# Kernel tuning notes

Hardware: AMD Instinct MI355X
Metric: run time of the kernel (lower is better)

## Reference

```python
import jax, jax.numpy as jnp
import numpy as np

B, L, DIM, H, D = 2, 2048, 1024, 16, 64


def setup_inputs() -> dict:
    key = jax.random.key(0)
    ks = jax.random.split(key, 20)
    s = 1.0 / np.sqrt(DIM)
    inp = {
        "query": jax.random.normal(ks[0], (B, L, DIM), jnp.float32),
        "keys": jax.random.normal(ks[1], (B, L, DIM), jnp.float32),
        "values": jax.random.normal(ks[2], (B, L, DIM), jnp.float32),
        "focus_vector": jax.random.normal(ks[3], (B, DIM), jnp.float32),
        "temporal_weights": jax.random.normal(ks[4], (B, L), jnp.float32),
        "importance_weights": jax.random.normal(ks[5], (B, L), jnp.float32),
        # linear params, stored [in, out] for x @ W + b
        "Wq": jax.random.normal(ks[6], (DIM, H * D), jnp.float32) * s,
        "bq": jnp.zeros((H * D,), jnp.float32),
        "Wk": jax.random.normal(ks[7], (DIM, H * D), jnp.float32) * s,
        "bk": jnp.zeros((H * D,), jnp.float32),
        "Wv": jax.random.normal(ks[8], (DIM, H * D), jnp.float32) * s,
        "bv": jnp.zeros((H * D,), jnp.float32),
        "Wp": jax.random.normal(ks[9], (H * D, DIM), jnp.float32) * s,
        "bp": jnp.zeros((DIM,), jnp.float32),
        "Wt": jax.random.normal(ks[10], (DIM, 1), jnp.float32) * s,
        "bt": jnp.zeros((1,), jnp.float32),
        "Wi": jax.random.normal(ks[11], (DIM, 1), jnp.float32) * s,
        "bi": jnp.zeros((1,), jnp.float32),
    }
    return inp


def reference(query, keys, values, focus_vector, temporal_weights, importance_weights,
              Wq, bq, Wk, bk, Wv, bv, Wp, bp, Wt, bt, Wi, bi):
    b, l, _ = query.shape
    # QKV projections -> [B, H, L, D]
    q = (query @ Wq + bq).reshape(b, l, H, D).transpose(0, 2, 1, 3)
    k = (keys @ Wk + bk).reshape(b, -1, H, D).transpose(0, 2, 1, 3)
    v = (values @ Wv + bv).reshape(b, -1, H, D).transpose(0, 2, 1, 3)
    scores = jnp.einsum("bhqd,bhkd->bhqk", q, k) / np.sqrt(D).astype(np.float32)
    # gate-modulated weights over keys [B, Lk]
    temporal_scores = (keys @ Wt + bt)[..., 0]
    tw = jax.nn.softmax(temporal_scores * temporal_weights, axis=-1)
    importance_scores = (keys @ Wi + bi)[..., 0]
    iw = jax.nn.softmax(importance_scores * importance_weights, axis=-1)
    rw = jax.nn.softmax(jnp.einsum("bkd,bd->bk", keys, focus_vector), axis=-1)
    combined = (tw + iw + rw) / 3.0
    scores = scores * combined[:, None, None, :]
    weights = jax.nn.softmax(scores, axis=-1)  # dropout is identity in eval
    out = jnp.einsum("bhqk,bhkd->bhqd", weights, v)
    out = out.transpose(0, 2, 1, 3).reshape(b, l, H * D)
    out = out @ Wp + bp
    return out, weights
```

## Files before the change

kernel.cpp:

```cpp
#include <hip/hip_runtime.h>
#include <hip/hip_bf16.h>
#include <cstdint>

#define DEV static __device__ __forceinline__

typedef __attribute__((ext_vector_type(8))) short short8_;
typedef __attribute__((ext_vector_type(4))) float float4_;
typedef __attribute__((ext_vector_type(4))) float f4v;
typedef __attribute__((ext_vector_type(4))) unsigned short u16x4;
typedef unsigned short u16;

constexpr int Bb   = 2;
constexpr int Ls   = 2048;
constexpr int DIMc = 1024;
constexpr int Hh   = 16;
constexpr int Dd   = 64;
constexpr int BL   = Bb * Ls;
constexpr int HD   = Hh * Dd;

DEV u16 f2bf(float f) {
  union { float f; uint32_t u; } v; v.f = f;
  return (u16)((v.u + 0x7fffu + ((v.u >> 16) & 1u)) >> 16);
}

DEV float4_ mfma16(short8_ a, short8_ b, float4_ c) {
  return __builtin_amdgcn_mfma_f32_16x16x32_bf16(a, b, c, 0, 0, 0);
}

DEV void gload_lds16(const void* g, void* l) {
  __builtin_amdgcn_global_load_lds(
      (const __attribute__((address_space(1))) void*)g,
      (__attribute__((address_space(3))) void*)l, 16, 0, 0);
}

__global__ void k_cast(const float* __restrict__ src, u16* __restrict__ dst, int n4) {
  int i = blockIdx.x * 256 + threadIdx.x;
  if (i >= n4) return;
  f4v v = ((const f4v*)src)[i];
  u16x4 o = { f2bf(v[0]), f2bf(v[1]), f2bf(v[2]), f2bf(v[3]) };
  ((u16x4*)dst)[i] = o;
}

__global__ void k_trans(const float* __restrict__ W, u16* __restrict__ WT) {
  __shared__ float t[64][65];
  int tx = threadIdx.x & 63;
  int tg = threadIdx.x >> 6;
  int n0 = blockIdx.x * 64;
  int k0 = blockIdx.y * 64;
#pragma unroll
  for (int i = 0; i < 16; ++i) {
    int r = tg * 16 + i;
    t[r][tx] = W[(size_t)(k0 + r) * HD + n0 + tx];
  }
  __syncthreads();
#pragma unroll
  for (int i = 0; i < 16; ++i) {
    int r = tg * 16 + i;
    WT[(size_t)(n0 + r) * DIMc + k0 + tx] = f2bf(t[tx][r]);
  }
}

__global__ void k_gates(const float* __restrict__ keys, const float* __restrict__ Wt,
                        const float* __restrict__ bt, const float* __restrict__ Wi,
                        const float* __restrict__ bi, const float* __restrict__ focus,
                        float* __restrict__ ts, float* __restrict__ is_, float* __restrict__ rs) {
  int wv = threadIdx.x >> 6, ln = threadIdx.x & 63;
  int row = blockIdx.x * 4 + wv;
  int b = row >> 11;
  const float* kr = keys + (size_t)row * DIMc;
  const float* fr = focus + (size_t)b * DIMc;
  float st = 0.f, si = 0.f, sr = 0.f;
  for (int j = ln; j < DIMc; j += 64) {
    float kv = kr[j];
    st += kv * Wt[j]; si += kv * Wi[j]; sr += kv * fr[j];
  }
#pragma unroll
  for (int m = 1; m < 64; m <<= 1) {
    st += __shfl_xor(st, m); si += __shfl_xor(si, m); sr += __shfl_xor(sr, m);
  }
  if (ln == 0) { ts[row] = st + bt[0]; is_[row] = si + bi[0]; rs[row] = sr; }
}

__global__ void k_combined(const float* __restrict__ ts, const float* __restrict__ is_,
                           const float* __restrict__ rs, const float* __restrict__ tw,
                           const float* __restrict__ iw, float* __restrict__ comb) {
  int b = blockIdx.x, t = threadIdx.x;
  __shared__ float red[3][4];
  float lt[8], li[8], lr[8];
  float m3[3] = {-1e30f, -1e30f, -1e30f};
#pragma unroll
  for (int i = 0; i < 8; ++i) {
    int gi = b * Ls + i * 256 + t;
    lt[i] = ts[gi] * tw[gi];
    li[i] = is_[gi] * iw[gi];
    lr[i] = rs[gi];
    m3[0] = fmaxf(m3[0], lt[i]); m3[1] = fmaxf(m3[1], li[i]); m3[2] = fmaxf(m3[2], lr[i]);
  }
#pragma unroll
  for (int q = 0; q < 3; ++q) {
    float v = m3[q];
#pragma unroll
    for (int m = 32; m; m >>= 1) v = fmaxf(v, __shfl_xor(v, m));
    if ((t & 63) == 0) red[q][t >> 6] = v;
  }
  __syncthreads();
#pragma unroll
  for (int q = 0; q < 3; ++q)
    m3[q] = fmaxf(fmaxf(red[q][0], red[q][1]), fmaxf(red[q][2], red[q][3]));
  __syncthreads();
  float s3[3] = {0.f, 0.f, 0.f};
#pragma unroll
  for (int i = 0; i < 8; ++i) {
    lt[i] = __expf(lt[i] - m3[0]); s3[0] += lt[i];
    li[i] = __expf(li[i] - m3[1]); s3[1] += li[i];
    lr[i] = __expf(lr[i] - m3[2]); s3[2] += lr[i];
  }
#pragma unroll
  for (int q = 0; q < 3; ++q) {
    float v = s3[q];
#pragma unroll
    for (int m = 32; m; m >>= 1) v += __shfl_xor(v, m);
    if ((t & 63) == 0) red[q][t >> 6] = v;
  }
  __syncthreads();
#pragma unroll
  for (int q = 0; q < 3; ++q) s3[q] = red[q][0] + red[q][1] + red[q][2] + red[q][3];
  float rt = 1.f / s3[0], ri = 1.f / s3[1], rr = 1.f / s3[2];
  const float third = 1.f / 3.f;
#pragma unroll
  for (int i = 0; i < 8; ++i) {
    int gi = b * Ls + i * 256 + t;
    comb[gi] = (lt[i] * rt + li[i] * ri + lr[i] * rr) * third;
  }
}

template <int MODE>
__launch_bounds__(256, 2)
__global__ void k_gemm(const u16* __restrict__ A, const u16* __restrict__ BT,
                       const float* __restrict__ bias, void* __restrict__ out) {
  __shared__ __align__(16) u16 As[128 * 32];
  __shared__ __align__(16) u16 Bs[128 * 32];
  const int tid = threadIdx.x, wv = tid >> 6, ln = tid & 63;
  const int g = ln >> 4, c = ln & 15;
  const int m0 = blockIdx.x * 128, n0 = blockIdx.y * 128;
  const int wm = wv >> 1, wn = wv & 1;
  const float4_ z4 = {0.f, 0.f, 0.f, 0.f};
  float4_ acc[4][4];
#pragma unroll
  for (int i = 0; i < 4; ++i)
#pragma unroll
    for (int j = 0; j < 4; ++j) acc[i][j] = z4;
  const int lrow = ln >> 2, lcol = (ln & 3) * 8;
  for (int k0 = 0; k0 < 1024; k0 += 32) {
#pragma unroll
    for (int s = 0; s < 2; ++s) {
      int r0 = wv * 32 + s * 16;
      gload_lds16(A  + (size_t)(m0 + r0 + lrow) * 1024 + k0 + lcol, &As[r0 * 32]);
      gload_lds16(BT + (size_t)(n0 + r0 + lrow) * 1024 + k0 + lcol, &Bs[r0 * 32]);
    }
    __syncthreads();
    short8_ af[4], bfr[4];
#pragma unroll
    for (int mt = 0; mt < 4; ++mt)
      af[mt] = *(const short8_*)&As[(wm * 64 + mt * 16 + c) * 32 + g * 8];
#pragma unroll
    for (int nt = 0; nt < 4; ++nt)
      bfr[nt] = *(const short8_*)&Bs[(wn * 64 + nt * 16 + c) * 32 + g * 8];
#pragma unroll
    for (int mt = 0; mt < 4; ++mt)
#pragma unroll
      for (int nt = 0; nt < 4; ++nt)
        acc[mt][nt] = mfma16(af[mt], bfr[nt], acc[mt][nt]);
    __syncthreads();
  }
  if constexpr (MODE == 3) {
    float* O = (float*)out;
#pragma unroll
    for (int mt = 0; mt < 4; ++mt)
#pragma unroll
      for (int nt = 0; nt < 4; ++nt) {
        int n = n0 + wn * 64 + nt * 16 + c;
        float bv = bias[n];
#pragma unroll
        for (int r = 0; r < 4; ++r) {
          int m = m0 + wm * 64 + mt * 16 + g * 4 + r;
          O[(size_t)m * HD + n] = acc[mt][nt][r] + bv;
        }
      }
  } else if constexpr (MODE == 2) {
    u16* vT = (u16*)out;
#pragma unroll
    for (int mt = 0; mt < 4; ++mt)
#pragma unroll
      for (int nt = 0; nt < 4; ++nt) {
        int n = n0 + wn * 64 + nt * 16 + c;
        float bv = bias[n];
        int h = n >> 6, d = n & 63;
        int mrow = m0 + wm * 64 + mt * 16 + g * 4;
        int b = mrow >> 11, l = mrow & 2047;
        u16x4 o = { f2bf(acc[mt][nt][0] + bv), f2bf(acc[mt][nt][1] + bv),
                    f2bf(acc[mt][nt][2] + bv), f2bf(acc[mt][nt][3] + bv) };
        *(u16x4*)&vT[((size_t)((b * Hh + h) * Dd + d)) * Ls + l] = o;
      }
  } else {
    u16* Q = (u16*)out;
#pragma unroll
    for (int mt = 0; mt < 4; ++mt)
#pragma unroll
      for (int nt = 0; nt < 4; ++nt) {
        int n = n0 + wn * 64 + nt * 16 + c;
        float bv = bias[n];
        int h = n >> 6, d = n & 63;
#pragma unroll
        for (int r = 0; r < 4; ++r) {
          int m = m0 + wm * 64 + mt * 16 + g * 4 + r;
          int b = m >> 11, l = m & 2047;
          Q[((size_t)((b * Hh + h) * Ls + l)) * Dd + d] = f2bf(acc[mt][nt][r] + bv);
        }
      }
  }
}

__launch_bounds__(256, 3)
__global__ void k_attn2(const u16* __restrict__ q_bh, const u16* __restrict__ k_bh,
                        const u16* __restrict__ vT, const float* __restrict__ comb_g,
                        float* __restrict__ wout, u16* __restrict__ ctx) {
  __shared__ __align__(16) u16 Kt[2][64][64];
  __shared__ __align__(16) u16 Vt[2][64][64];
  __shared__ float comb[Ls];
  __shared__ __align__(16) u16 e_w[4][16][72];
  __shared__ float inv_w[4][16];

  const int bid = blockIdx.x;
  const int logical = (bid & 7) * 128 + (bid >> 3);
  const int bh = logical >> 5, qb = logical & 31;
  const int b = bh >> 4, h = bh & 15;
  const int l0 = qb * 64;
  const int w = threadIdx.x >> 6, ln = threadIdx.x & 63;
  const int g = ln >> 4, c = ln & 15;
  const int srow = ln >> 3, x8 = ln & 7;
  const float4_ z4 = {0.f, 0.f, 0.f, 0.f};

  const u16* kbh = k_bh + (size_t)bh * Ls * Dd;
  const u16* vbh = vT + (size_t)bh * Dd * Ls;

  const u16* qp = q_bh + ((size_t)bh * Ls + l0 + w * 16) * Dd;
  short8_ aq0 = *(const short8_*)&qp[c * Dd + g * 8];
  short8_ aq1 = *(const short8_*)&qp[c * Dd + 32 + g * 8];

  auto stageK = [&](int buf, int kb) {
#pragma unroll
    for (int i = 0; i < 2; ++i) {
      int rr = w * 16 + i * 8 + srow;
      int sc = (x8 ^ (rr & 7)) * 8;
      gload_lds16(kbh + (size_t)(kb + rr) * Dd + sc, &Kt[buf][w * 16 + i * 8][0]);
    }
  };
  auto stageV = [&](int buf, int kb) {
#pragma unroll
    for (int i = 0; i < 2; ++i) {
      int rr = w * 16 + i * 8 + srow;
      int sc = (x8 ^ (rr & 7)) * 8;
      gload_lds16(vbh + (size_t)rr * Ls + kb + sc, &Vt[buf][w * 16 + i * 8][0]);
    }
  };

  float4_ accO[4];
#pragma unroll
  for (int dt = 0; dt < 4; ++dt) accO[dt] = z4;
  float rsum4[4] = {0.f, 0.f, 0.f, 0.f};

  stageK(0, 0); stageV(0, 0);
  for (int i = threadIdx.x; i < Ls; i += 256) comb[i] = comb_g[b * Ls + i] * 0.125f;
  __syncthreads();

  int buf = 0;
  for (int t = 0; t < 32; ++t) {
    if (t < 31) { stageK(buf ^ 1, (t + 1) * 64); stageV(buf ^ 1, (t + 1) * 64); }
    const int kb = t * 64;
#pragma unroll
    for (int s = 0; s < 4; ++s) {
      int rowK = s * 16 + c;
      short8_ bk0 = *(const short8_*)&Kt[buf][rowK][((g    ) ^ (c & 7)) * 8];
      short8_ bk1 = *(const short8_*)&Kt[buf][rowK][((4 + g) ^ (c & 7)) * 8];
      float4_ st = mfma16(aq0, bk0, z4);
      st = mfma16(aq1, bk1, st);
      float cc = comb[kb + rowK];
#pragma unroll
      for (int r = 0; r < 4; ++r) {
        float e = __expf(st[r] * cc);
        rsum4[r] += e;
        e_w[w][g * 4 + r][s * 16 + c] = f2bf(e);
      }
    }
#pragma unroll
    for (int hf = 0; hf < 2; ++hf) {
      short8_ ea = *(const short8_*)&e_w[w][c][hf * 32 + g * 8];
#pragma unroll
      for (int dt = 0; dt < 4; ++dt) {
        short8_ bv = *(const short8_*)&Vt[buf][dt * 16 + c][((hf * 4 + g) ^ (c & 7)) * 8];
        accO[dt] = mfma16(ea, bv, accO[dt]);
      }
    }
    __syncthreads();
    buf ^= 1;
  }

#pragma unroll
  for (int m = 1; m < 16; m <<= 1)
#pragma unroll
    for (int r = 0; r < 4; ++r) rsum4[r] += __shfl_xor(rsum4[r], m);
  float invr[4];
#pragma unroll
  for (int r = 0; r < 4; ++r) invr[r] = 1.0f / rsum4[r];
  if (c == 0)
#pragma unroll
    for (int r = 0; r < 4; ++r) inv_w[w][g * 4 + r] = invr[r];

  u16* out_lds = &Vt[0][0][0] + w * 1152;
#pragma unroll
  for (int dt = 0; dt < 4; ++dt)
#pragma unroll
    for (int r = 0; r < 4; ++r)
      out_lds[(g * 4 + r) * 72 + dt * 16 + c] = f2bf(accO[dt][r] * invr[r]);
  {
    int rr2 = ln >> 2, sg = ln & 3;
    short8_ d0 = *(const short8_*)&out_lds[rr2 * 72 + sg * 16];
    short8_ d1 = *(const short8_*)&out_lds[rr2 * 72 + sg * 16 + 8];
    u16* cp = ctx + ((size_t)(b * Ls + l0 + w * 16 + rr2)) * HD + h * Dd + sg * 16;
    *(short8_*)cp = d0;
    *(short8_*)(cp + 8) = d1;
  }

  float ivq = inv_w[w][c];
  stageK(0, 0);
  __syncthreads();
  buf = 0;
  float* wb = wout + ((size_t)bh * Ls + l0 + w * 16) * Ls;
  for (int t = 0; t < 32; ++t) {
    if (t < 31) stageK(buf ^ 1, (t + 1) * 64);
    const int kb = t * 64;
#pragma unroll
    for (int s = 0; s < 4; ++s) {
      int rowK = s * 16 + c;
      short8_ bk0 = *(const short8_*)&Kt[buf][rowK][((g    ) ^ (c & 7)) * 8];
      short8_ bk1 = *(const short8_*)&Kt[buf][rowK][((4 + g) ^ (c & 7)) * 8];
      float4_ st = mfma16(bk0, aq0, z4);
      st = mfma16(bk1, aq1, st);
      float4_ cc4 = *(const float4_*)&comb[kb + s * 16 + g * 4];
      float4_ o;
#pragma unroll
      for (int r = 0; r < 4; ++r) o[r] = __expf(st[r] * cc4[r]) * ivq;
      *(float4_*)&wb[(size_t)c * Ls + kb + s * 16 + g * 4] = o;
    }
    __syncthreads();
    buf ^= 1;
  }
}

extern "C" void kernel_launch(void* const* d_in, const int* in_sizes, int n_in,
                              void* d_out, int out_size, void* d_ws, size_t ws_size,
                              hipStream_t stream) {
  (void)in_sizes; (void)n_in; (void)out_size; (void)ws_size;
  const float* query = (const float*)d_in[0];
  const float* keys  = (const float*)d_in[1];
  const float* values= (const float*)d_in[2];
  const float* focus = (const float*)d_in[3];
  const float* twg   = (const float*)d_in[4];
  const float* iwg   = (const float*)d_in[5];
  const float* Wq = (const float*)d_in[6];  const float* bq = (const float*)d_in[7];
  const float* Wk = (const float*)d_in[8];  const float* bk = (const float*)d_in[9];
  const float* Wv = (const float*)d_in[10]; const float* bv = (const float*)d_in[11];
  const float* Wp = (const float*)d_in[12]; const float* bp = (const float*)d_in[13];
  const float* Wt = (const float*)d_in[14]; const float* bt = (const float*)d_in[15];
  const float* Wi = (const float*)d_in[16]; const float* bi = (const float*)d_in[17];

  char* ws = (char*)d_ws;
  size_t off = 0;
  auto alloc = [&](size_t bytes) -> char* {
    char* p = ws + off; off += (bytes + 255) & ~(size_t)255; return p;
  };
  const size_t NTOK = (size_t)BL * DIMc;
  u16* qx   = (u16*)alloc(NTOK * 2);
  u16* kx   = (u16*)alloc(NTOK * 2);
  u16* vx   = (u16*)alloc(NTOK * 2);
  u16* WqT  = (u16*)alloc((size_t)DIMc * HD * 2);
  u16* WkT  = (u16*)alloc((size_t)DIMc * HD * 2);
  u16* WvT  = (u16*)alloc((size_t)DIMc * HD * 2);
  u16* WpT  = (u16*)alloc((size_t)DIMc * HD * 2);
  u16* q_bh = (u16*)alloc(NTOK * 2);
  u16* k_bh = (u16*)alloc(NTOK * 2);
  u16* vTb  = (u16*)alloc(NTOK * 2);
  u16* ctx  = (u16*)alloc(NTOK * 2);
  float* ts   = (float*)alloc((size_t)BL * 4);
  float* is_  = (float*)alloc((size_t)BL * 4);
  float* rs   = (float*)alloc((size_t)BL * 4);
  float* comb = (float*)alloc((size_t)BL * 4);

  float* out_f = (float*)d_out;
  float* w_out = out_f + (size_t)BL * HD;

  const int n4 = (int)(NTOK / 4);
  k_cast<<<4096, 256, 0, stream>>>(query,  qx, n4);
  k_cast<<<4096, 256, 0, stream>>>(keys,   kx, n4);
  k_cast<<<4096, 256, 0, stream>>>(values, vx, n4);
  dim3 tg(16, 16);
  k_trans<<<tg, 256, 0, stream>>>(Wq, WqT);
  k_trans<<<tg, 256, 0, stream>>>(Wk, WkT);
  k_trans<<<tg, 256, 0, stream>>>(Wv, WvT);
  k_trans<<<tg, 256, 0, stream>>>(Wp, WpT);
  k_gates<<<1024, 256, 0, stream>>>(keys, Wt, bt, Wi, bi, focus, ts, is_, rs);
  k_combined<<<2, 256, 0, stream>>>(ts, is_, rs, twg, iwg, comb);
  dim3 gg(32, 8);
  k_gemm<0><<<gg, 256, 0, stream>>>(qx, WqT, bq, q_bh);
  k_gemm<0><<<gg, 256, 0, stream>>>(kx, WkT, bk, k_bh);
  k_gemm<2><<<gg, 256, 0, stream>>>(vx, WvT, bv, vTb);
  k_attn2<<<1024, 256, 0, stream>>>(q_bh, k_bh, vTb, comb, w_out, ctx);
  k_gemm<3><<<gg, 256, 0, stream>>>(ctx, WpT, bp, out_f);
}
```

Baseline: 341.5 us.

## Batch cast, transpose and QKV GEMM launches; trim attention LDS and swizzle

New measurement: 297.6 us. 12.9% less time.

```diff
diff --git a/kernel.cpp b/kernel.cpp
--- a/kernel.cpp
+++ b/kernel.cpp
@@ -33,16 +33,26 @@
       (__attribute__((address_space(3))) void*)l, 16, 0, 0);
 }
 
-__global__ void k_cast(const float* __restrict__ src, u16* __restrict__ dst, int n4) {
+__global__ void k_cast3(const float* __restrict__ a, const float* __restrict__ b,
+                        const float* __restrict__ c, u16* __restrict__ oa,
+                        u16* __restrict__ ob, u16* __restrict__ oc) {
+  int z = blockIdx.y;
+  const float* s = (z == 0) ? a : (z == 1) ? b : c;
+  u16* d = (z == 0) ? oa : (z == 1) ? ob : oc;
   int i = blockIdx.x * 256 + threadIdx.x;
-  if (i >= n4) return;
-  f4v v = ((const f4v*)src)[i];
+  f4v v = ((const f4v*)s)[i];
   u16x4 o = { f2bf(v[0]), f2bf(v[1]), f2bf(v[2]), f2bf(v[3]) };
-  ((u16x4*)dst)[i] = o;
-}
-
-__global__ void k_trans(const float* __restrict__ W, u16* __restrict__ WT) {
+  ((u16x4*)d)[i] = o;
+}
+
+__global__ void k_trans4(const float* __restrict__ W0, const float* __restrict__ W1,
+                         const float* __restrict__ W2, const float* __restrict__ W3,
+                         u16* __restrict__ T0, u16* __restrict__ T1,
+                         u16* __restrict__ T2, u16* __restrict__ T3) {
   __shared__ float t[64][65];
+  int z = blockIdx.z;
+  const float* W = (z == 0) ? W0 : (z == 1) ? W1 : (z == 2) ? W2 : W3;
+  u16* WT = (z == 0) ? T0 : (z == 1) ? T1 : (z == 2) ? T2 : T3;
   int tx = threadIdx.x & 63;
   int tg = threadIdx.x >> 6;
   int n0 = blockIdx.x * 64;
@@ -126,20 +136,27 @@
 #pragma unroll
   for (int q = 0; q < 3; ++q) s3[q] = red[q][0] + red[q][1] + red[q][2] + red[q][3];
   float rt = 1.f / s3[0], ri = 1.f / s3[1], rr = 1.f / s3[2];
-  const float third = 1.f / 3.f;
+  const float scl = (1.f / 3.f) * 0.125f;
 #pragma unroll
   for (int i = 0; i < 8; ++i) {
     int gi = b * Ls + i * 256 + t;
-    comb[gi] = (lt[i] * rt + li[i] * ri + lr[i] * rr) * third;
-  }
-}
-
-template <int MODE>
+    comb[gi] = (lt[i] * rt + li[i] * ri + lr[i] * rr) * scl;
+  }
+}
+
 __launch_bounds__(256, 2)
-__global__ void k_gemm(const u16* __restrict__ A, const u16* __restrict__ BT,
-                       const float* __restrict__ bias, void* __restrict__ out) {
+__global__ void k_gemm_qkv(const u16* __restrict__ qx, const u16* __restrict__ kx,
+                           const u16* __restrict__ vx, const u16* __restrict__ WqT,
+                           const u16* __restrict__ WkT, const u16* __restrict__ WvT,
+                           const float* __restrict__ bq, const float* __restrict__ bk,
+                           const float* __restrict__ bv, u16* __restrict__ q_bh,
+                           u16* __restrict__ k_bh, u16* __restrict__ vT) {
   __shared__ __align__(16) u16 As[128 * 32];
   __shared__ __align__(16) u16 Bs[128 * 32];
+  const int z = blockIdx.z;
+  const u16* A  = (z == 0) ? qx : (z == 1) ? kx : vx;
+  const u16* BT = (z == 0) ? WqT : (z == 1) ? WkT : WvT;
+  const float* bias = (z == 0) ? bq : (z == 1) ? bk : bv;
   const int tid = threadIdx.x, wv = tid >> 6, ln = tid & 63;
   const int g = ln >> 4, c = ln & 15;
   const int m0 = blockIdx.x * 128, n0 = blockIdx.y * 128;
@@ -173,63 +190,98 @@
         acc[mt][nt] = mfma16(af[mt], bfr[nt], acc[mt][nt]);
     __syncthreads();
   }
-  if constexpr (MODE == 3) {
-    float* O = (float*)out;
+  if (z < 2) {
+    u16* Q = (z == 0) ? q_bh : k_bh;
 #pragma unroll
     for (int mt = 0; mt < 4; ++mt)
 #pragma unroll
       for (int nt = 0; nt < 4; ++nt) {
         int n = n0 + wn * 64 + nt * 16 + c;
-        float bv = bias[n];
+        float bv_ = bias[n];
+        int h = n >> 6, d = n & 63;
 #pragma unroll
         for (int r = 0; r < 4; ++r) {
           int m = m0 + wm * 64 + mt * 16 + g * 4 + r;
-          O[(size_t)m * HD + n] = acc[mt][nt][r] + bv;
+          int b = m >> 11, l = m & 2047;
+          Q[((size_t)((b * Hh + h) * Ls + l)) * Dd + d] = f2bf(acc[mt][nt][r] + bv_);
         }
       }
-  } else if constexpr (MODE == 2) {
-    u16* vT = (u16*)out;
+  } else {
 #pragma unroll
     for (int mt = 0; mt < 4; ++mt)
 #pragma unroll
       for (int nt = 0; nt < 4; ++nt) {
         int n = n0 + wn * 64 + nt * 16 + c;
-        float bv = bias[n];
+        float bv_ = bias[n];
         int h = n >> 6, d = n & 63;
         int mrow = m0 + wm * 64 + mt * 16 + g * 4;
         int b = mrow >> 11, l = mrow & 2047;
-        u16x4 o = { f2bf(acc[mt][nt][0] + bv), f2bf(acc[mt][nt][1] + bv),
-                    f2bf(acc[mt][nt][2] + bv), f2bf(acc[mt][nt][3] + bv) };
+        u16x4 o = { f2bf(acc[mt][nt][0] + bv_), f2bf(acc[mt][nt][1] + bv_),
+                    f2bf(acc[mt][nt][2] + bv_), f2bf(acc[mt][nt][3] + bv_) };
         *(u16x4*)&vT[((size_t)((b * Hh + h) * Dd + d)) * Ls + l] = o;
       }
-  } else {
-    u16* Q = (u16*)out;
-#pragma unroll
-    for (int mt = 0; mt < 4; ++mt)
-#pragma unroll
-      for (int nt = 0; nt < 4; ++nt) {
-        int n = n0 + wn * 64 + nt * 16 + c;
-        float bv = bias[n];
-        int h = n >> 6, d = n & 63;
-#pragma unroll
-        for (int r = 0; r < 4; ++r) {
-          int m = m0 + wm * 64 + mt * 16 + g * 4 + r;
-          int b = m >> 11, l = m & 2047;
-          Q[((size_t)((b * Hh + h) * Ls + l)) * Dd + d] = f2bf(acc[mt][nt][r] + bv);
-        }
+  }
+}
+
+__launch_bounds__(256, 4)
+__global__ void k_gemmO(const u16* __restrict__ A, const u16* __restrict__ BT,
+                        const float* __restrict__ bias, float* __restrict__ O) {
+  __shared__ __align__(16) u16 As[64 * 32];
+  __shared__ __align__(16) u16 Bs[128 * 32];
+  const int tid = threadIdx.x, wv = tid >> 6, ln = tid & 63;
+  const int g = ln >> 4, c = ln & 15;
+  const int m0 = blockIdx.x * 64, n0 = blockIdx.y * 128;
+  const int wm = wv >> 1, wn = wv & 1;
+  const float4_ z4 = {0.f, 0.f, 0.f, 0.f};
+  float4_ acc[2][4];
+#pragma unroll
+  for (int i = 0; i < 2; ++i)
+#pragma unroll
+    for (int j = 0; j < 4; ++j) acc[i][j] = z4;
+  const int lrow = ln >> 2, lcol = (ln & 3) * 8;
+  for (int k0 = 0; k0 < 1024; k0 += 32) {
+    gload_lds16(A + (size_t)(m0 + wv * 16 + lrow) * 1024 + k0 + lcol, &As[(wv * 16) * 32]);
+#pragma unroll
+    for (int s = 0; s < 2; ++s) {
+      int r0 = wv * 32 + s * 16;
+      gload_lds16(BT + (size_t)(n0 + r0 + lrow) * 1024 + k0 + lcol, &Bs[r0 * 32]);
+    }
+    __syncthreads();
+    short8_ af[2], bfr[4];
+#pragma unroll
+    for (int mt = 0; mt < 2; ++mt)
+      af[mt] = *(const short8_*)&As[(wm * 32 + mt * 16 + c) * 32 + g * 8];
+#pragma unroll
+    for (int nt = 0; nt < 4; ++nt)
+      bfr[nt] = *(const short8_*)&Bs[(wn * 64 + nt * 16 + c) * 32 + g * 8];
+#pragma unroll
+    for (int mt = 0; mt < 2; ++mt)
+#pragma unroll
+      for (int nt = 0; nt < 4; ++nt)
+        acc[mt][nt] = mfma16(af[mt], bfr[nt], acc[mt][nt]);
+    __syncthreads();
+  }
+#pragma unroll
+  for (int mt = 0; mt < 2; ++mt)
+#pragma unroll
+    for (int nt = 0; nt < 4; ++nt) {
+      int n = n0 + wn * 64 + nt * 16 + c;
+      float bv_ = bias[n];
+#pragma unroll
+      for (int r = 0; r < 4; ++r) {
+        int m = m0 + wm * 32 + mt * 16 + g * 4 + r;
+        O[(size_t)m * HD + n] = acc[mt][nt][r] + bv_;
       }
-  }
-}
-
-__launch_bounds__(256, 3)
-__global__ void k_attn2(const u16* __restrict__ q_bh, const u16* __restrict__ k_bh,
+    }
+}
+
+__launch_bounds__(256, 4)
+__global__ void k_attn3(const u16* __restrict__ q_bh, const u16* __restrict__ k_bh,
                         const u16* __restrict__ vT, const float* __restrict__ comb_g,
                         float* __restrict__ wout, u16* __restrict__ ctx) {
   __shared__ __align__(16) u16 Kt[2][64][64];
   __shared__ __align__(16) u16 Vt[2][64][64];
-  __shared__ float comb[Ls];
-  __shared__ __align__(16) u16 e_w[4][16][72];
-  __shared__ float inv_w[4][16];
+  __shared__ __align__(16) u16 e_w[4][16][64];
 
   const int bid = blockIdx.x;
   const int logical = (bid & 7) * 128 + (bid >> 3);
@@ -243,6 +295,7 @@
 
   const u16* kbh = k_bh + (size_t)bh * Ls * Dd;
   const u16* vbh = vT + (size_t)bh * Dd * Ls;
+  const float* kcomb = comb_g + (size_t)b * Ls;
 
   const u16* qp = q_bh + ((size_t)bh * Ls + l0 + w * 16) * Dd;
   short8_ aq0 = *(const short8_*)&qp[c * Dd + g * 8];
@@ -271,7 +324,6 @@
   float rsum4[4] = {0.f, 0.f, 0.f, 0.f};
 
   stageK(0, 0); stageV(0, 0);
-  for (int i = threadIdx.x; i < Ls; i += 256) comb[i] = comb_g[b * Ls + i] * 0.125f;
   __syncthreads();
 
   int buf = 0;
@@ -285,17 +337,19 @@
       short8_ bk1 = *(const short8_*)&Kt[buf][rowK][((4 + g) ^ (c & 7)) * 8];
       float4_ st = mfma16(aq0, bk0, z4);
       st = mfma16(aq1, bk1, st);
-      float cc = comb[kb + rowK];
+      float cc = kcomb[kb + rowK];
+      int chunk0 = s * 2 + (c >> 3), w7 = c & 7;
 #pragma unroll
       for (int r = 0; r < 4; ++r) {
         float e = __expf(st[r] * cc);
         rsum4[r] += e;
-        e_w[w][g * 4 + r][s * 16 + c] = f2bf(e);
+        int row = g * 4 + r;
+        e_w[w][row][((chunk0 ^ (row & 7)) << 3) | w7] = f2bf(e);
       }
     }
 #pragma unroll
     for (int hf = 0; hf < 2; ++hf) {
-      short8_ ea = *(const short8_*)&e_w[w][c][hf * 32 + g * 8];
+      short8_ ea = *(const short8_*)&e_w[w][c][(((hf * 4 + g) ^ (c & 7)) << 3)];
 #pragma unroll
       for (int dt = 0; dt < 4; ++dt) {
         short8_ bv = *(const short8_*)&Vt[buf][dt * 16 + c][((hf * 4 + g) ^ (c & 7)) * 8];
@@ -313,9 +367,10 @@
   float invr[4];
 #pragma unroll
   for (int r = 0; r < 4; ++r) invr[r] = 1.0f / rsum4[r];
+  float* ivp = (float*)&e_w[w][0][0];
   if (c == 0)
 #pragma unroll
-    for (int r = 0; r < 4; ++r) inv_w[w][g * 4 + r] = invr[r];
+    for (int r = 0; r < 4; ++r) ivp[g * 4 + r] = invr[r];
 
   u16* out_lds = &Vt[0][0][0] + w * 1152;
 #pragma unroll
@@ -332,7 +387,7 @@
     *(short8_*)(cp + 8) = d1;
   }
 
-  float ivq = inv_w[w][c];
+  float ivq = ivp[c];
   stageK(0, 0);
   __syncthreads();
   buf = 0;
@@ -347,7 +402,7 @@
       short8_ bk1 = *(const short8_*)&Kt[buf][rowK][((4 + g) ^ (c & 7)) * 8];
       float4_ st = mfma16(bk0, aq0, z4);
       st = mfma16(bk1, aq1, st);
-      float4_ cc4 = *(const float4_*)&comb[kb + s * 16 + g * 4];
+      float4_ cc4 = *(const float4_*)&kcomb[kb + s * 16 + g * 4];
       float4_ o;
 #pragma unroll
       for (int r = 0; r < 4; ++r) o[r] = __expf(st[r] * cc4[r]) * ivq;
@@ -400,21 +455,16 @@
   float* out_f = (float*)d_out;
   float* w_out = out_f + (size_t)BL * HD;
 
-  const int n4 = (int)(NTOK / 4);
-  k_cast<<<4096, 256, 0, stream>>>(query,  qx, n4);
-  k_cast<<<4096, 256, 0, stream>>>(keys,   kx, n4);
-  k_cast<<<4096, 256, 0, stream>>>(values, vx, n4);
-  dim3 tg(16, 16);
-  k_trans<<<tg, 256, 0, stream>>>(Wq, WqT);
-  k_trans<<<tg, 256, 0, stream>>>(Wk, WkT);
-  k_trans<<<tg, 256, 0, stream>>>(Wv, WvT);
-  k_trans<<<tg, 256, 0, stream>>>(Wp, WpT);
+  dim3 cg(4096, 3);
+  k_cast3<<<cg, 256, 0, stream>>>(query, keys, values, qx, kx, vx);
+  dim3 tg(16, 16, 4);
+  k_trans4<<<tg, 256, 0, stream>>>(Wq, Wk, Wv, Wp, WqT, WkT, WvT, WpT);
   k_gates<<<1024, 256, 0, stream>>>(keys, Wt, bt, Wi, bi, focus, ts, is_, rs);
   k_combined<<<2, 256, 0, stream>>>(ts, is_, rs, twg, iwg, comb);
-  dim3 gg(32, 8);
-  k_gemm<0><<<gg, 256, 0, stream>>>(qx, WqT, bq, q_bh);
-  k_gemm<0><<<gg, 256, 0, stream>>>(kx, WkT, bk, k_bh);
-  k_gemm<2><<<gg, 256, 0, stream>>>(vx, WvT, bv, vTb);
-  k_attn2<<<1024, 256, 0, stream>>>(q_bh, k_bh, vTb, comb, w_out, ctx);
-  k_gemm<3><<<gg, 256, 0, stream>>>(ctx, WpT, bp, out_f);
-}
+  dim3 gq(32, 8, 3);
+  k_gemm_qkv<<<gq, 256, 0, stream>>>(qx, kx, vx, WqT, WkT, WvT, bq, bk, bv,
+                                     q_bh, k_bh, vTb);
+  k_attn3<<<1024, 256, 0, stream>>>(q_bh, k_bh, vTb, comb, w_out, ctx);
+  dim3 go(64, 8);
+  k_gemmO<<<go, 256, 0, stream>>>(ctx, WpT, bp, out_f);
+}
```
